# Kernel optimization log

Measured on AMD Instinct MI355X. Metric: run time of the kernel, lower is better.

The kernel has to match this reference:

```python
import jax, jax.numpy as jnp
import numpy as np

N = 100000        # num nodes
E = 3_200_000     # num edges
NFEAT, NHID, NCLASS = 256, 128, 40
BN_EPS = 1e-5


def _gcn_norm(edge_index, edge_weight, num_nodes):
    """PyG gcn_norm with self-loops (fill value 1.0): returns (src, dst, norm)."""
    loop = jnp.arange(num_nodes)
    src = jnp.concatenate([edge_index[0], loop])
    dst = jnp.concatenate([edge_index[1], loop])
    ew = jnp.concatenate([edge_weight, jnp.ones((num_nodes,), edge_weight.dtype)])
    deg = jax.ops.segment_sum(ew, dst, num_segments=num_nodes)
    dinv = jnp.where(deg > 0, jax.lax.rsqrt(jnp.maximum(deg, 1e-30)), 0.0)
    norm = dinv[src] * ew * dinv[dst]  # [E+N]
    return src, dst, norm


def _gcn_layer(h, W, b, src, dst, norm, num_nodes):
    lin = h @ W                                   # [N, out]
    msg = lin[src] * norm[:, None]                # gather + scale  [E+N, out]
    agg = jax.ops.segment_sum(msg, dst, num_segments=num_nodes)
    return agg + b


def _bn(h, gamma, beta):
    # BatchNorm1d in training mode: biased batch statistics
    m = jnp.mean(h, axis=0)
    v = jnp.mean(jnp.square(h - m), axis=0)
    return (h - m) * jax.lax.rsqrt(v + BN_EPS) * gamma + beta


def setup_inputs() -> dict:
    key = jax.random.key(0)
    ks = jax.random.split(key, 12)
    s_in = 1.0 / np.sqrt(NFEAT)
    s_h = 1.0 / np.sqrt(NHID)
    return {
        "x": jax.random.normal(ks[0], (N, NFEAT), jnp.float32),
        "edge_index": jax.random.randint(ks[1], (2, E), 0, N, dtype=jnp.int32),
        "edge_weight": jax.random.uniform(ks[2], (E,), jnp.float32),
        "W1": jax.random.normal(ks[3], (NFEAT, NHID), jnp.float32) * s_in,
        "b1": jnp.zeros((NHID,), jnp.float32),
        "g1": jnp.ones((NHID,), jnp.float32),
        "beta1": jnp.zeros((NHID,), jnp.float32),
        "W2": jax.random.normal(ks[4], (NHID, NHID), jnp.float32) * s_h,
        "b2": jnp.zeros((NHID,), jnp.float32),
        "g2": jnp.ones((NHID,), jnp.float32),
        "beta2": jnp.zeros((NHID,), jnp.float32),
        "W3": jax.random.normal(ks[5], (NHID, NHID), jnp.float32) * s_h,
        "b3": jnp.zeros((NHID,), jnp.float32),
        "g3": jnp.ones((NHID,), jnp.float32),
        "beta3": jnp.zeros((NHID,), jnp.float32),
        "linW": jax.random.normal(ks[6], (3 * NHID, NCLASS), jnp.float32) / np.sqrt(3 * NHID),
        "linb": jnp.zeros((NCLASS,), jnp.float32),
    }


def reference(x, edge_index, edge_weight,
              W1, b1, g1, beta1,
              W2, b2, g2, beta2,
              W3, b3, g3, beta3,
              linW, linb):
    src, dst, norm = _gcn_norm(edge_index, edge_weight, N)
    x1 = _bn(jax.nn.relu(_gcn_layer(x, W1, b1, src, dst, norm, N)), g1, beta1)
    x2 = _bn(jax.nn.relu(_gcn_layer(x1, W2, b2, src, dst, norm, N)), g2, beta2)
    x3 = _bn(_gcn_layer(x2, W3, b3, src, dst, norm, N), g3, beta3)  # note: no relu on x3
    embed_x = jnp.concatenate([x1, x2, x3], axis=1)  # [N, 3*NHID]
    logits = embed_x @ linW + linb                   # [N, NCLASS]
    return logits, jax.nn.softmax(logits, axis=1), embed_x
```

## Files before the change

### kernel.cpp

```cpp
#include <hip/hip_runtime.h>
#include <hip/hip_bf16.h>
#include <hip/hip_fp16.h>
#include <math.h>

#define NN 100000
#define NE 3200000
#define NF 256
#define NH 128
#define NC 40
#define BN_EPS 1e-5f

typedef __attribute__((ext_vector_type(8))) short bf16x8;
typedef __attribute__((ext_vector_type(4))) float f32x4;

__device__ __forceinline__ float2 bf2_unpack(unsigned int v) {
    return make_float2(__uint_as_float(v << 16), __uint_as_float(v & 0xffff0000u));
}
__device__ __forceinline__ unsigned int pack2bf(float lo, float hi) {
    unsigned int a = (unsigned int)__hip_bfloat16_raw(__float2bfloat16(lo)).x;
    unsigned int b = (unsigned int)__hip_bfloat16_raw(__float2bfloat16(hi)).x;
    return a | (b << 16);
}
__device__ __forceinline__ float4 affine4(float4 v, float4 sc, float4 sh) {
    v.x = fmaf(v.x, sc.x, sh.x);
    v.y = fmaf(v.y, sc.y, sh.y);
    v.z = fmaf(v.z, sc.z, sh.z);
    v.w = fmaf(v.w, sc.w, sh.w);
    return v;
}

__global__ __launch_bounds__(256) void k_init(unsigned long long* hist, float* sums) {
    int i = blockIdx.x * 256 + threadIdx.x;
    if (i < NN) hist[i] = 0ULL;
    if (i < 3 * 1024) sums[i] = 0.0f;
}

template <int K, bool BN>
__device__ __forceinline__ void gemm_body(unsigned int (*Bt)[20], const float* H, float* Hw,
                                          const float* scsh, int ldh, const float* W,
                                          __hip_bfloat16* out, int blk, int t) {
    int wid = t >> 6, l = t & 63;
    int l15 = l & 15, lhi = l >> 4;
    int rowbase = blk * 128 + wid * 32;
    int ar0 = rowbase + l15;      if (ar0 >= NN) ar0 = NN - 1;
    int ar1 = rowbase + 16 + l15; if (ar1 >= NN) ar1 = NN - 1;

    f32x4 acc[2][8];
#pragma unroll
    for (int rt = 0; rt < 2; rt++)
#pragma unroll
        for (int ct = 0; ct < 8; ct++) acc[rt][ct] = (f32x4){0.f, 0.f, 0.f, 0.f};

    for (int kb = 0; kb < K / 32; kb++) {
        __syncthreads();
        for (int i = t; i < 2048; i += 256) {
            int c = i & 127, k2l = i >> 7;
            int k = kb * 32 + 2 * k2l;
            Bt[c][k2l] = pack2bf(W[(size_t)k * NH + c], W[(size_t)(k + 1) * NH + c]);
        }
        __syncthreads();
        int kk = kb * 32 + lhi * 8;
        const float4* a0p = (const float4*)&H[(size_t)ar0 * ldh + kk];
        const float4* a1p = (const float4*)&H[(size_t)ar1 * ldh + kk];
        float4 x0 = a0p[0], x1 = a0p[1];
        float4 y0 = a1p[0], y1 = a1p[1];
        if constexpr (BN) {
            float4 sc0 = *(const float4*)&scsh[kk];
            float4 sc1 = *(const float4*)&scsh[kk + 4];
            float4 sh0 = *(const float4*)&scsh[128 + kk];
            float4 sh1 = *(const float4*)&scsh[128 + kk + 4];
            x0 = affine4(x0, sc0, sh0); x1 = affine4(x1, sc1, sh1);
            y0 = affine4(y0, sc0, sh0); y1 = affine4(y1, sc1, sh1);
            *(float4*)&Hw[(size_t)ar0 * ldh + kk] = x0;
            *(float4*)&Hw[(size_t)ar0 * ldh + kk + 4] = x1;
            *(float4*)&Hw[(size_t)ar1 * ldh + kk] = y0;
            *(float4*)&Hw[(size_t)ar1 * ldh + kk + 4] = y1;
        }
        union { unsigned int u[4]; bf16x8 v; } af0, af1;
        af0.u[0] = pack2bf(x0.x, x0.y); af0.u[1] = pack2bf(x0.z, x0.w);
        af0.u[2] = pack2bf(x1.x, x1.y); af0.u[3] = pack2bf(x1.z, x1.w);
        af1.u[0] = pack2bf(y0.x, y0.y); af1.u[1] = pack2bf(y0.z, y0.w);
        af1.u[2] = pack2bf(y1.x, y1.y); af1.u[3] = pack2bf(y1.z, y1.w);
#pragma unroll
        for (int ct = 0; ct < 8; ct++) {
            bf16x8 b = *(const bf16x8*)&Bt[ct * 16 + l15][lhi * 4];
            acc[0][ct] = __builtin_amdgcn_mfma_f32_16x16x32_bf16(af0.v, b, acc[0][ct], 0, 0, 0);
            acc[1][ct] = __builtin_amdgcn_mfma_f32_16x16x32_bf16(af1.v, b, acc[1][ct], 0, 0, 0);
        }
    }
#pragma unroll
    for (int rt = 0; rt < 2; rt++)
#pragma unroll
        for (int ct = 0; ct < 8; ct++)
#pragma unroll
            for (int reg = 0; reg < 4; reg++) {
                int row = rowbase + rt * 16 + lhi * 4 + reg;
                if (row < NN)
                    out[(size_t)row * NH + ct * 16 + l15] = __float2bfloat16(acc[rt][ct][reg]);
            }
}

__global__ __launch_bounds__(256) void k_g1edge(const float* __restrict__ x, const float* __restrict__ W1,
                                                __hip_bfloat16* __restrict__ lin,
                                                const int* __restrict__ ei, const float* __restrict__ ew,
                                                unsigned long long* __restrict__ hist,
                                                int* __restrict__ pos, int gm) {
    __shared__ unsigned int Bt[128][20];
    int t = threadIdx.x;
    int blk = (int)blockIdx.x;
    if (blk < gm) {
        gemm_body<NF, false>(Bt, x, nullptr, nullptr, NF, W1, lin, blk, t);
    } else {
        int e = (blk - gm) * 256 + t;
        if (e < NE) {
            int d = __builtin_nontemporal_load(&ei[NE + e]);
            float w = __builtin_nontemporal_load(&ew[e]);
            unsigned long long pk = (1ULL << 44) | (unsigned long long)(w * 4294967296.0f);
            unsigned long long old = atomicAdd(&hist[d], pk);
            __builtin_nontemporal_store((int)(old >> 44), &pos[e]);
        }
    }
}

__global__ __launch_bounds__(256) void k_gemm_bn(const float* H, float* Hw,
                                                 const float* __restrict__ scsh,
                                                 const float* __restrict__ W,
                                                 __hip_bfloat16* __restrict__ out) {
    __shared__ unsigned int Bt[128][20];
    gemm_body<NH, true>(Bt, H, Hw, scsh, 384, W, out, (int)blockIdx.x, (int)threadIdx.x);
}

__global__ __launch_bounds__(256) void k_dinv(const unsigned long long* __restrict__ hist,
                                              float* __restrict__ dinv) {
    int i = blockIdx.x * 256 + threadIdx.x;
    if (i < NN) {
        float ws = (float)(hist[i] & 0xFFFFFFFFFFFULL) * 2.3283064365386963e-10f;
        dinv[i] = rsqrtf(1.0f + ws);
    }
}

__global__ __launch_bounds__(1024) void k_scan(const unsigned long long* __restrict__ hist,
                                               int* __restrict__ rowptr) {
    __shared__ int wsum[16];
    __shared__ int s_carry;
    int t = threadIdx.x;
    int lane = t & 63, wid = t >> 6;
    if (t == 0) s_carry = 0;
    __syncthreads();
    for (int base = 0; base < NN; base += 4096) {
        int i0 = base + t * 4;
        int c[4];
#pragma unroll
        for (int j = 0; j < 4; j++) {
            int i = i0 + j;
            c[j] = (i < NN) ? (int)(hist[i] >> 44) : 0;
        }
        int v = c[0] + c[1] + c[2] + c[3];
        int x = v;
#pragma unroll
        for (int off = 1; off < 64; off <<= 1) {
            int y = __shfl_up(x, off);
            if (lane >= off) x += y;
        }
        if (lane == 63) wsum[wid] = x;
        __syncthreads();
        if (wid == 0 && lane < 16) {
            int s = wsum[lane];
#pragma unroll
            for (int off = 1; off < 16; off <<= 1) {
                int y = __shfl_up(s, off);
                if (lane >= off) s += y;
            }
            wsum[lane] = s;
        }
        __syncthreads();
        int woff = (wid > 0) ? wsum[wid - 1] : 0;
        int incl = x + woff;
        int carry = s_carry;
        int run = carry + incl - v;
#pragma unroll
        for (int j = 0; j < 4; j++) {
            int i = i0 + j;
            if (i < NN) rowptr[i] = run;
            run += c[j];
        }
        __syncthreads();
        if (t == 1023) s_carry = carry + incl;
        __syncthreads();
    }
    if (t == 0) rowptr[NN] = s_carry;
}

__global__ __launch_bounds__(256) void k_scatter(const int* __restrict__ ei, const float* __restrict__ ew,
                                                 const float* __restrict__ dinv,
                                                 const int* __restrict__ rowptr,
                                                 const int* __restrict__ pos,
                                                 unsigned int* __restrict__ cw) {
    int e = blockIdx.x * 256 + threadIdx.x;
    if (e >= NE) return;
    int s = __builtin_nontemporal_load(&ei[e]);
    int d = __builtin_nontemporal_load(&ei[NE + e]);
    float w = __builtin_nontemporal_load(&ew[e]);
    float nv = dinv[s] * w * dinv[d];
    unsigned int h = (unsigned int)__half_as_ushort(__float2half(nv)) & 0x7fffu;
    unsigned int packed = (unsigned int)s | (h << 17);
    int p = __builtin_nontemporal_load(&pos[e]);
    __builtin_nontemporal_store(packed, &cw[rowptr[d] + p]);
}

__global__ __launch_bounds__(256) void k_agg(const unsigned int* __restrict__ linb,
                                             const float* __restrict__ dinv,
                                             const int* __restrict__ rowptr,
                                             const unsigned int* __restrict__ cw,
                                             const float* __restrict__ bias,
                                             float* __restrict__ outp, int do_relu) {
    int t = threadIdx.x;
    int node = blockIdx.x * 4 + (t >> 6);
    if (node >= NN) return;
    int ch = t & 63;
    int c = ch << 1;
    float di = dinv[node];
    float2 sv = bf2_unpack(linb[(size_t)node * 64 + ch]);
    float a0 = fmaf(sv.x, di * di, bias[c]);
    float a1 = fmaf(sv.y, di * di, bias[c + 1]);
    int beg = rowptr[node], end = rowptr[node + 1];
    int j = beg;
    for (; j + 16 <= end; j += 16) {
        unsigned int pk[16];
#pragma unroll
        for (int q = 0; q < 16; q++) pk[q] = cw[j + q];
        unsigned int v[16];
#pragma unroll
        for (int q = 0; q < 16; q++) v[q] = linb[(size_t)(pk[q] & 0x1FFFFu) * 64 + ch];
#pragma unroll
        for (int q = 0; q < 16; q++) {
            float w = __half2float(__ushort_as_half((unsigned short)(pk[q] >> 17)));
            float2 f = bf2_unpack(v[q]);
            a0 = fmaf(f.x, w, a0);
            a1 = fmaf(f.y, w, a1);
        }
    }
    for (; j + 4 <= end; j += 4) {
        unsigned int pk[4];
#pragma unroll
        for (int q = 0; q < 4; q++) pk[q] = cw[j + q];
        unsigned int v[4];
#pragma unroll
        for (int q = 0; q < 4; q++) v[q] = linb[(size_t)(pk[q] & 0x1FFFFu) * 64 + ch];
#pragma unroll
        for (int q = 0; q < 4; q++) {
            float w = __half2float(__ushort_as_half((unsigned short)(pk[q] >> 17)));
            float2 f = bf2_unpack(v[q]);
            a0 = fmaf(f.x, w, a0);
            a1 = fmaf(f.y, w, a1);
        }
    }
    for (; j < end; j++) {
        unsigned int pk = cw[j];
        unsigned int vv = linb[(size_t)(pk & 0x1FFFFu) * 64 + ch];
        float w = __half2float(__ushort_as_half((unsigned short)(pk >> 17)));
        float2 f = bf2_unpack(vv);
        a0 = fmaf(f.x, w, a0);
        a1 = fmaf(f.y, w, a1);
    }
    if (do_relu) { a0 = fmaxf(a0, 0.f); a1 = fmaxf(a1, 0.f); }
    *(float2*)&outp[(size_t)node * 384 + c] = make_float2(a0, a1);
}

__global__ __launch_bounds__(256) void k_stats(const float* __restrict__ pre, float* __restrict__ sums) {
    int t = threadIdx.x;
    int c = t & 127, h = t >> 7;
    float s = 0.f, s2 = 0.f;
    for (int r = blockIdx.x * 2 + h; r < NN; r += gridDim.x * 2) {
        float v = pre[(size_t)r * 384 + c];
        s += v;
        s2 = fmaf(v, v, s2);
    }
    __shared__ float ls[256], ls2[256];
    ls[t] = s; ls2[t] = s2;
    __syncthreads();
    if (t < 128) {
        atomicAdd(&sums[c], ls[t] + ls[t + 128]);
        atomicAdd(&sums[NH + c], ls2[t] + ls2[t + 128]);
    }
}

__global__ void k_bnfinal(float* __restrict__ sums, const float* __restrict__ g,
                          const float* __restrict__ beta) {
    int c = threadIdx.x;
    if (c < NH) {
        float m = sums[c] * (1.0f / NN);
        float v = sums[NH + c] * (1.0f / NN) - m * m;
        float rstd = rsqrtf(v + BN_EPS);
        float sc = g[c] * rstd;
        sums[256 + c] = sc;
        sums[384 + c] = beta[c] - m * sc;
    }
}

__global__ __launch_bounds__(256) void k_final(const float* __restrict__ embed, float* embedW,
                                               const float* __restrict__ scsh3,
                                               const float* __restrict__ linW,
                                               const float* __restrict__ linb,
                                               float* __restrict__ logits, float* __restrict__ probs) {
    __shared__ unsigned int Wt[3 * 16 * 196];
    int t = threadIdx.x;
    for (int i = t; i < 3 * 16 * 192; i += 256) {
        int ct = i / (16 * 192);
        int rem = i - ct * (16 * 192);
        int c = rem / 192, k2 = rem - c * 192;
        int col = ct * 16 + c;
        float lo = (col < NC) ? linW[(size_t)(2 * k2) * NC + col] : 0.f;
        float hi = (col < NC) ? linW[(size_t)(2 * k2 + 1) * NC + col] : 0.f;
        Wt[(ct * 16 + c) * 196 + k2] = pack2bf(lo, hi);
    }
    __syncthreads();

    int wid = t >> 6, l = t & 63;
    int rowbase = blockIdx.x * 64 + wid * 16;
    int l15 = l & 15, lhi = l >> 4;

    int arow = rowbase + l15;
    if (arow > NN - 1) arow = NN - 1;
    const float4* ap = (const float4*)&embed[(size_t)arow * 384 + lhi * 8];

    f32x4 acc0 = {0.f, 0.f, 0.f, 0.f};
    f32x4 acc1 = {0.f, 0.f, 0.f, 0.f};
    f32x4 acc2 = {0.f, 0.f, 0.f, 0.f};

    for (int kb = 0; kb < 12; kb++) {
        float4 a0 = ap[kb * 8];
        float4 a1 = ap[kb * 8 + 1];
        if (kb >= 8) {
            int kk = kb * 32 + lhi * 8 - 256;
            float4 sc0 = *(const float4*)&scsh3[kk];
            float4 sc1 = *(const float4*)&scsh3[kk + 4];
            float4 sh0 = *(const float4*)&scsh3[128 + kk];
            float4 sh1 = *(const float4*)&scsh3[128 + kk + 4];
            a0 = affine4(a0, sc0, sh0);
            a1 = affine4(a1, sc1, sh1);
            *(float4*)&embedW[(size_t)arow * 384 + kb * 32 + lhi * 8] = a0;
            *(float4*)&embedW[(size_t)arow * 384 + kb * 32 + lhi * 8 + 4] = a1;
        }
        union { unsigned int u[4]; bf16x8 v; } af;
        af.u[0] = pack2bf(a0.x, a0.y);
        af.u[1] = pack2bf(a0.z, a0.w);
        af.u[2] = pack2bf(a1.x, a1.y);
        af.u[3] = pack2bf(a1.z, a1.w);
        int wbase = kb * 16 + lhi * 4;
        bf16x8 b0 = *(const bf16x8*)&Wt[(0 * 16 + l15) * 196 + wbase];
        bf16x8 b1 = *(const bf16x8*)&Wt[(1 * 16 + l15) * 196 + wbase];
        bf16x8 b2 = *(const bf16x8*)&Wt[(2 * 16 + l15) * 196 + wbase];
        acc0 = __builtin_amdgcn_mfma_f32_16x16x32_bf16(af.v, b0, acc0, 0, 0, 0);
        acc1 = __builtin_amdgcn_mfma_f32_16x16x32_bf16(af.v, b1, acc1, 0, 0, 0);
        acc2 = __builtin_amdgcn_mfma_f32_16x16x32_bf16(af.v, b2, acc2, 0, 0, 0);
    }

    int col0 = 0 * 16 + l15, col1 = 1 * 16 + l15, col2 = 2 * 16 + l15;
    float lb0 = (col0 < NC) ? linb[col0] : 0.f;
    float lb1 = (col1 < NC) ? linb[col1] : 0.f;
    float lb2 = (col2 < NC) ? linb[col2] : 0.f;

#pragma unroll
    for (int reg = 0; reg < 4; reg++) {
        int row = rowbase + lhi * 4 + reg;
        float v0 = acc0[reg] + lb0;
        float v1 = acc1[reg] + lb1;
        float v2 = acc2[reg] + lb2;
        float m = fmaxf(v0, v1);
        if (col2 < NC) m = fmaxf(m, v2);
#pragma unroll
        for (int off = 1; off < 16; off <<= 1) m = fmaxf(m, __shfl_xor(m, off));
        float e0 = __expf(v0 - m);
        float e1 = __expf(v1 - m);
        float e2 = (col2 < NC) ? __expf(v2 - m) : 0.f;
        float s = e0 + e1 + e2;
#pragma unroll
        for (int off = 1; off < 16; off <<= 1) s += __shfl_xor(s, off);
        float inv = 1.0f / s;
        if (row < NN) {
            size_t base = (size_t)row * NC;
            logits[base + col0] = v0;
            probs[base + col0] = e0 * inv;
            logits[base + col1] = v1;
            probs[base + col1] = e1 * inv;
            if (col2 < NC) {
                logits[base + col2] = v2;
                probs[base + col2] = e2 * inv;
            }
        }
    }
}

extern "C" void kernel_launch(void* const* d_in, const int* in_sizes, int n_in,
                              void* d_out, int out_size, void* d_ws, size_t ws_size,
                              hipStream_t stream) {
    const float* x    = (const float*)d_in[0];
    const int*   ei   = (const int*)d_in[1];
    const float* ew   = (const float*)d_in[2];
    const float* W1   = (const float*)d_in[3];
    const float* b1   = (const float*)d_in[4];
    const float* g1   = (const float*)d_in[5];
    const float* be1  = (const float*)d_in[6];
    const float* W2   = (const float*)d_in[7];
    const float* b2   = (const float*)d_in[8];
    const float* g2   = (const float*)d_in[9];
    const float* be2  = (const float*)d_in[10];
    const float* W3   = (const float*)d_in[11];
    const float* b3   = (const float*)d_in[12];
    const float* g3   = (const float*)d_in[13];
    const float* be3  = (const float*)d_in[14];
    const float* linW = (const float*)d_in[15];
    const float* linb = (const float*)d_in[16];

    float* out    = (float*)d_out;
    float* logits = out;
    float* probs  = out + (size_t)NN * NC;
    float* embed  = out + (size_t)2 * NN * NC;

    char* ws = (char*)d_ws;
    size_t off = 0;
    auto alloc = [&](size_t bytes) -> char* {
        char* p = ws + off;
        off = (off + bytes + 255) & ~(size_t)255;
        return p;
    };
    float*              dinv   = (float*)alloc((size_t)NN * 4);
    unsigned long long* hist   = (unsigned long long*)alloc((size_t)NN * 8);
    int*                rowptr = (int*)alloc((size_t)(NN + 1) * 4);
    unsigned int*       cw     = (unsigned int*)alloc((size_t)NE * 4);
    __hip_bfloat16*     lin    = (__hip_bfloat16*)alloc((size_t)NN * NH * 2);
    int*                pos    = (int*)alloc((size_t)NE * 4);
    float*              sums   = (float*)alloc(3 * 1024 * 4);
    (void)ws_size; (void)in_sizes; (void)n_in; (void)out_size;

    int gN = (NN + 255) / 256;
    int gE = (NE + 255) / 256;
    int gM = (NN + 127) / 128;
    int gA = (NN + 3) / 4;
    int gF = (NN + 63) / 64;

    k_init<<<gN, 256, 0, stream>>>(hist, sums);
    k_g1edge<<<gM + gE, 256, 0, stream>>>(x, W1, lin, ei, ew, hist, pos, gM);
    k_dinv<<<gN, 256, 0, stream>>>(hist, dinv);
    k_scan<<<1, 1024, 0, stream>>>(hist, rowptr);
    k_scatter<<<gE, 256, 0, stream>>>(ei, ew, dinv, rowptr, pos, cw);

    k_agg<<<gA, 256, 0, stream>>>((const unsigned int*)lin, dinv, rowptr, cw, b1, embed + 0, 1);
    k_stats<<<1024, 256, 0, stream>>>(embed + 0, sums + 0);
    k_bnfinal<<<1, 128, 0, stream>>>(sums + 0, g1, be1);
    k_gemm_bn<<<gM, 256, 0, stream>>>(embed + 0, embed + 0, sums + 256, W2, lin);
    k_agg<<<gA, 256, 0, stream>>>((const unsigned int*)lin, dinv, rowptr, cw, b2, embed + 128, 1);
    k_stats<<<1024, 256, 0, stream>>>(embed + 128, sums + 1024);
    k_bnfinal<<<1, 128, 0, stream>>>(sums + 1024, g2, be2);
    k_gemm_bn<<<gM, 256, 0, stream>>>(embed + 128, embed + 128, sums + 1024 + 256, W3, lin);
    k_agg<<<gA, 256, 0, stream>>>((const unsigned int*)lin, dinv, rowptr, cw, b3, embed + 256, 0);
    k_stats<<<1024, 256, 0, stream>>>(embed + 256, sums + 2048);
    k_bnfinal<<<1, 128, 0, stream>>>(sums + 2048, g3, be3);
    k_final<<<gF, 256, 0, stream>>>(embed, embed, sums + 2048 + 256, linW, linb, logits, probs);
}
```

Measured before the change: 989.6 us.

## Split aggregation into two channel-half passes with edge-parallel half-waves

The SpMM aggregation now runs as two launches, each covering half the 128 channels, so each pass gathers 64-byte slices of the bf16 feature rows. Within a wavefront, the two half-waves process alternating edges and combine their sums with a cross-lane shuffle. The intent is a smaller gather working set per pass, which should fit better in cache, plus more memory parallelism per node. The cost is reading the CSR edge list twice and doubling the agg launches. Separately, the dinv computation moves into the scan kernel, and the edge histogram is split out of the fused GEMM1+edge kernel so that GEMM1 runs after the scatter.

```diff
diff --git a/kernel.cpp b/kernel.cpp
--- a/kernel.cpp
+++ b/kernel.cpp
@@ -33,6 +33,93 @@
     int i = blockIdx.x * 256 + threadIdx.x;
     if (i < NN) hist[i] = 0ULL;
     if (i < 3 * 1024) sums[i] = 0.0f;
+}
+
+__global__ __launch_bounds__(256) void k_edge(const int* __restrict__ ei, const float* __restrict__ ew,
+                                              unsigned long long* __restrict__ hist,
+                                              int* __restrict__ pos) {
+    int e = blockIdx.x * 256 + threadIdx.x;
+    if (e >= NE) return;
+    int d = __builtin_nontemporal_load(&ei[NE + e]);
+    float w = __builtin_nontemporal_load(&ew[e]);
+    unsigned long long pack = (1ULL << 44) | (unsigned long long)(w * 4294967296.0f);
+    unsigned long long old = atomicAdd(&hist[d], pack);
+    __builtin_nontemporal_store((int)(old >> 44), &pos[e]);
+}
+
+__global__ __launch_bounds__(1024) void k_scan(const unsigned long long* __restrict__ hist,
+                                               int* __restrict__ rowptr,
+                                               float* __restrict__ dinv) {
+    __shared__ int wsum[16];
+    __shared__ int s_carry;
+    int t = threadIdx.x;
+    int lane = t & 63, wid = t >> 6;
+    if (t == 0) s_carry = 0;
+    __syncthreads();
+    for (int base = 0; base < NN; base += 4096) {
+        int i0 = base + t * 4;
+        int c[4];
+#pragma unroll
+        for (int j = 0; j < 4; j++) {
+            int i = i0 + j;
+            unsigned long long h = (i < NN) ? hist[i] : 0ULL;
+            c[j] = (int)(h >> 44);
+            if (i < NN) {
+                float ws = (float)(h & 0xFFFFFFFFFFFULL) * 2.3283064365386963e-10f;
+                dinv[i] = rsqrtf(1.0f + ws);
+            }
+        }
+        int v = c[0] + c[1] + c[2] + c[3];
+        int x = v;
+#pragma unroll
+        for (int off = 1; off < 64; off <<= 1) {
+            int y = __shfl_up(x, off);
+            if (lane >= off) x += y;
+        }
+        if (lane == 63) wsum[wid] = x;
+        __syncthreads();
+        if (wid == 0 && lane < 16) {
+            int s = wsum[lane];
+#pragma unroll
+            for (int off = 1; off < 16; off <<= 1) {
+                int y = __shfl_up(s, off);
+                if (lane >= off) s += y;
+            }
+            wsum[lane] = s;
+        }
+        __syncthreads();
+        int woff = (wid > 0) ? wsum[wid - 1] : 0;
+        int incl = x + woff;
+        int carry = s_carry;
+        int run = carry + incl - v;
+#pragma unroll
+        for (int j = 0; j < 4; j++) {
+            int i = i0 + j;
+            if (i < NN) rowptr[i] = run;
+            run += c[j];
+        }
+        __syncthreads();
+        if (t == 1023) s_carry = carry + incl;
+        __syncthreads();
+    }
+    if (t == 0) rowptr[NN] = s_carry;
+}
+
+__global__ __launch_bounds__(256) void k_scatter(const int* __restrict__ ei, const float* __restrict__ ew,
+                                                 const float* __restrict__ dinv,
+                                                 const int* __restrict__ rowptr,
+                                                 const int* __restrict__ pos,
+                                                 unsigned int* __restrict__ cw) {
+    int e = blockIdx.x * 256 + threadIdx.x;
+    if (e >= NE) return;
+    int s = __builtin_nontemporal_load(&ei[e]);
+    int d = __builtin_nontemporal_load(&ei[NE + e]);
+    float w = __builtin_nontemporal_load(&ew[e]);
+    float nv = dinv[s] * w * dinv[d];
+    unsigned int h = (unsigned int)__half_as_ushort(__float2half(nv)) & 0x7fffu;
+    unsigned int packed = (unsigned int)s | (h << 17);
+    int p = __builtin_nontemporal_load(&pos[e]);
+    __builtin_nontemporal_store(packed, &cw[rowptr[d] + p]);
 }
 
 template <int K, bool BN>
@@ -100,26 +187,11 @@
             }
 }
 
-__global__ __launch_bounds__(256) void k_g1edge(const float* __restrict__ x, const float* __restrict__ W1,
-                                                __hip_bfloat16* __restrict__ lin,
-                                                const int* __restrict__ ei, const float* __restrict__ ew,
-                                                unsigned long long* __restrict__ hist,
-                                                int* __restrict__ pos, int gm) {
+__global__ __launch_bounds__(256) void k_gemm1(const float* __restrict__ H,
+                                               const float* __restrict__ W,
+                                               __hip_bfloat16* __restrict__ out) {
     __shared__ unsigned int Bt[128][20];
-    int t = threadIdx.x;
-    int blk = (int)blockIdx.x;
-    if (blk < gm) {
-        gemm_body<NF, false>(Bt, x, nullptr, nullptr, NF, W1, lin, blk, t);
-    } else {
-        int e = (blk - gm) * 256 + t;
-        if (e < NE) {
-            int d = __builtin_nontemporal_load(&ei[NE + e]);
-            float w = __builtin_nontemporal_load(&ew[e]);
-            unsigned long long pk = (1ULL << 44) | (unsigned long long)(w * 4294967296.0f);
-            unsigned long long old = atomicAdd(&hist[d], pk);
-            __builtin_nontemporal_store((int)(old >> 44), &pos[e]);
-        }
-    }
+    gemm_body<NF, false>(Bt, H, nullptr, nullptr, NF, W, out, (int)blockIdx.x, (int)threadIdx.x);
 }
 
 __global__ __launch_bounds__(256) void k_gemm_bn(const float* H, float* Hw,
@@ -130,108 +202,39 @@
     gemm_body<NH, true>(Bt, H, Hw, scsh, 384, W, out, (int)blockIdx.x, (int)threadIdx.x);
 }
 
-__global__ __launch_bounds__(256) void k_dinv(const unsigned long long* __restrict__ hist,
-                                              float* __restrict__ dinv) {
-    int i = blockIdx.x * 256 + threadIdx.x;
-    if (i < NN) {
-        float ws = (float)(hist[i] & 0xFFFFFFFFFFFULL) * 2.3283064365386963e-10f;
-        dinv[i] = rsqrtf(1.0f + ws);
-    }
-}
-
-__global__ __launch_bounds__(1024) void k_scan(const unsigned long long* __restrict__ hist,
-                                               int* __restrict__ rowptr) {
-    __shared__ int wsum[16];
-    __shared__ int s_carry;
-    int t = threadIdx.x;
-    int lane = t & 63, wid = t >> 6;
-    if (t == 0) s_carry = 0;
-    __syncthreads();
-    for (int base = 0; base < NN; base += 4096) {
-        int i0 = base + t * 4;
-        int c[4];
-#pragma unroll
-        for (int j = 0; j < 4; j++) {
-            int i = i0 + j;
-            c[j] = (i < NN) ? (int)(hist[i] >> 44) : 0;
-        }
-        int v = c[0] + c[1] + c[2] + c[3];
-        int x = v;
-#pragma unroll
-        for (int off = 1; off < 64; off <<= 1) {
-            int y = __shfl_up(x, off);
-            if (lane >= off) x += y;
-        }
-        if (lane == 63) wsum[wid] = x;
-        __syncthreads();
-        if (wid == 0 && lane < 16) {
-            int s = wsum[lane];
-#pragma unroll
-            for (int off = 1; off < 16; off <<= 1) {
-                int y = __shfl_up(s, off);
-                if (lane >= off) s += y;
-            }
-            wsum[lane] = s;
-        }
-        __syncthreads();
-        int woff = (wid > 0) ? wsum[wid - 1] : 0;
-        int incl = x + woff;
-        int carry = s_carry;
-        int run = carry + incl - v;
-#pragma unroll
-        for (int j = 0; j < 4; j++) {
-            int i = i0 + j;
-            if (i < NN) rowptr[i] = run;
-            run += c[j];
-        }
-        __syncthreads();
-        if (t == 1023) s_carry = carry + incl;
-        __syncthreads();
-    }
-    if (t == 0) rowptr[NN] = s_carry;
-}
-
-__global__ __launch_bounds__(256) void k_scatter(const int* __restrict__ ei, const float* __restrict__ ew,
-                                                 const float* __restrict__ dinv,
-                                                 const int* __restrict__ rowptr,
-                                                 const int* __restrict__ pos,
-                                                 unsigned int* __restrict__ cw) {
-    int e = blockIdx.x * 256 + threadIdx.x;
-    if (e >= NE) return;
-    int s = __builtin_nontemporal_load(&ei[e]);
-    int d = __builtin_nontemporal_load(&ei[NE + e]);
-    float w = __builtin_nontemporal_load(&ew[e]);
-    float nv = dinv[s] * w * dinv[d];
-    unsigned int h = (unsigned int)__half_as_ushort(__float2half(nv)) & 0x7fffu;
-    unsigned int packed = (unsigned int)s | (h << 17);
-    int p = __builtin_nontemporal_load(&pos[e]);
-    __builtin_nontemporal_store(packed, &cw[rowptr[d] + p]);
-}
-
-__global__ __launch_bounds__(256) void k_agg(const unsigned int* __restrict__ linb,
-                                             const float* __restrict__ dinv,
-                                             const int* __restrict__ rowptr,
-                                             const unsigned int* __restrict__ cw,
-                                             const float* __restrict__ bias,
-                                             float* __restrict__ outp, int do_relu) {
+template <int PASS>
+__global__ __launch_bounds__(256) void k_agg_h(const unsigned int* __restrict__ linb,
+                                               const float* __restrict__ dinv,
+                                               const int* __restrict__ rowptr,
+                                               const unsigned int* __restrict__ cw,
+                                               const float* __restrict__ bias,
+                                               float* __restrict__ outp, int do_relu) {
     int t = threadIdx.x;
     int node = blockIdx.x * 4 + (t >> 6);
     if (node >= NN) return;
-    int ch = t & 63;
-    int c = ch << 1;
-    float di = dinv[node];
-    float2 sv = bf2_unpack(linb[(size_t)node * 64 + ch]);
-    float a0 = fmaf(sv.x, di * di, bias[c]);
-    float a1 = fmaf(sv.y, di * di, bias[c + 1]);
+    int lane = t & 63;
+    int epar = lane >> 5;
+    int ch32 = lane & 31;
+    int c = PASS * 64 + (ch32 << 1);
+    float a0, a1;
+    if (epar == 0) {
+        float di = dinv[node];
+        float2 sv = bf2_unpack(linb[(size_t)node * 64 + PASS * 32 + ch32]);
+        a0 = fmaf(sv.x, di * di, bias[c]);
+        a1 = fmaf(sv.y, di * di, bias[c + 1]);
+    } else {
+        a0 = 0.f; a1 = 0.f;
+    }
     int beg = rowptr[node], end = rowptr[node + 1];
     int j = beg;
-    for (; j + 16 <= end; j += 16) {
+    for (; j + 32 <= end; j += 32) {
         unsigned int pk[16];
 #pragma unroll
-        for (int q = 0; q < 16; q++) pk[q] = cw[j + q];
+        for (int q = 0; q < 16; q++) pk[q] = cw[j + 2 * q + epar];
         unsigned int v[16];
 #pragma unroll
-        for (int q = 0; q < 16; q++) v[q] = linb[(size_t)(pk[q] & 0x1FFFFu) * 64 + ch];
+        for (int q = 0; q < 16; q++)
+            v[q] = linb[(size_t)(pk[q] & 0x1FFFFu) * 64 + PASS * 32 + ch32];
 #pragma unroll
         for (int q = 0; q < 16; q++) {
             float w = __half2float(__ushort_as_half((unsigned short)(pk[q] >> 17)));
@@ -240,31 +243,28 @@
             a1 = fmaf(f.y, w, a1);
         }
     }
-    for (; j + 4 <= end; j += 4) {
-        unsigned int pk[4];
-#pragma unroll
-        for (int q = 0; q < 4; q++) pk[q] = cw[j + q];
-        unsigned int v[4];
-#pragma unroll
-        for (int q = 0; q < 4; q++) v[q] = linb[(size_t)(pk[q] & 0x1FFFFu) * 64 + ch];
-#pragma unroll
-        for (int q = 0; q < 4; q++) {
-            float w = __half2float(__ushort_as_half((unsigned short)(pk[q] >> 17)));
-            float2 f = bf2_unpack(v[q]);
-            a0 = fmaf(f.x, w, a0);
-            a1 = fmaf(f.y, w, a1);
-        }
-    }
-    for (; j < end; j++) {
-        unsigned int pk = cw[j];
-        unsigned int vv = linb[(size_t)(pk & 0x1FFFFu) * 64 + ch];
+    for (; j + 2 <= end; j += 2) {
+        unsigned int pk = cw[j + epar];
+        unsigned int vv = linb[(size_t)(pk & 0x1FFFFu) * 64 + PASS * 32 + ch32];
         float w = __half2float(__ushort_as_half((unsigned short)(pk >> 17)));
         float2 f = bf2_unpack(vv);
         a0 = fmaf(f.x, w, a0);
         a1 = fmaf(f.y, w, a1);
     }
-    if (do_relu) { a0 = fmaxf(a0, 0.f); a1 = fmaxf(a1, 0.f); }
-    *(float2*)&outp[(size_t)node * 384 + c] = make_float2(a0, a1);
+    if (j < end && epar == 0) {
+        unsigned int pk = cw[j];
+        unsigned int vv = linb[(size_t)(pk & 0x1FFFFu) * 64 + PASS * 32 + ch32];
+        float w = __half2float(__ushort_as_half((unsigned short)(pk >> 17)));
+        float2 f = bf2_unpack(vv);
+        a0 = fmaf(f.x, w, a0);
+        a1 = fmaf(f.y, w, a1);
+    }
+    a0 += __shfl_xor(a0, 32);
+    a1 += __shfl_xor(a1, 32);
+    if (epar == 0) {
+        if (do_relu) { a0 = fmaxf(a0, 0.f); a1 = fmaxf(a1, 0.f); }
+        *(float2*)&outp[(size_t)node * 384 + c] = make_float2(a0, a1);
+    }
 }
 
 __global__ __launch_bounds__(256) void k_stats(const float* __restrict__ pre, float* __restrict__ sums) {
@@ -441,20 +441,23 @@
     int gF = (NN + 63) / 64;
 
     k_init<<<gN, 256, 0, stream>>>(hist, sums);
-    k_g1edge<<<gM + gE, 256, 0, stream>>>(x, W1, lin, ei, ew, hist, pos, gM);
-    k_dinv<<<gN, 256, 0, stream>>>(hist, dinv);
-    k_scan<<<1, 1024, 0, stream>>>(hist, rowptr);
+    k_edge<<<gE, 256, 0, stream>>>(ei, ew, hist, pos);
+    k_scan<<<1, 1024, 0, stream>>>(hist, rowptr, dinv);
     k_scatter<<<gE, 256, 0, stream>>>(ei, ew, dinv, rowptr, pos, cw);
 
-    k_agg<<<gA, 256, 0, stream>>>((const unsigned int*)lin, dinv, rowptr, cw, b1, embed + 0, 1);
+    k_gemm1<<<gM, 256, 0, stream>>>(x, W1, lin);
+    k_agg_h<0><<<gA, 256, 0, stream>>>((const unsigned int*)lin, dinv, rowptr, cw, b1, embed + 0, 1);
+    k_agg_h<1><<<gA, 256, 0, stream>>>((const unsigned int*)lin, dinv, rowptr, cw, b1, embed + 0, 1);
     k_stats<<<1024, 256, 0, stream>>>(embed + 0, sums + 0);
     k_bnfinal<<<1, 128, 0, stream>>>(sums + 0, g1, be1);
     k_gemm_bn<<<gM, 256, 0, stream>>>(embed + 0, embed + 0, sums + 256, W2, lin);
-    k_agg<<<gA, 256, 0, stream>>>((const unsigned int*)lin, dinv, rowptr, cw, b2, embed + 128, 1);
+    k_agg_h<0><<<gA, 256, 0, stream>>>((const unsigned int*)lin, dinv, rowptr, cw, b2, embed + 128, 1);
+    k_agg_h<1><<<gA, 256, 0, stream>>>((const unsigned int*)lin, dinv, rowptr, cw, b2, embed + 128, 1);
     k_stats<<<1024, 256, 0, stream>>>(embed + 128, sums + 1024);
     k_bnfinal<<<1, 128, 0, stream>>>(sums + 1024, g2, be2);
     k_gemm_bn<<<gM, 256, 0, stream>>>(embed + 128, embed + 128, sums + 1024 + 256, W3, lin);
-    k_agg<<<gA, 256, 0, stream>>>((const unsigned int*)lin, dinv, rowptr, cw, b3, embed + 256, 0);
+    k_agg_h<0><<<gA, 256, 0, stream>>>((const unsigned int*)lin, dinv, rowptr, cw, b3, embed + 256, 0);
+    k_agg_h<1><<<gA, 256, 0, stream>>>((const unsigned int*)lin, dinv, rowptr, cw, b3, embed + 256, 0);
     k_stats<<<1024, 256, 0, stream>>>(embed + 256, sums + 2048);
     k_bnfinal<<<1, 128, 0, stream>>>(sums + 2048, g3, be3);
     k_final<<<gF, 256, 0, stream>>>(embed, embed, sums + 2048 + 256, linW, linb, logits, probs);
```

Result: slower. 1.342 ms (+35.7%).

## Split fused GEMM1/edge-histogram kernel and fold dinv into single-block scan

Applied to the files above, without the earlier changes.

Undoes the fusion of the first GEMM with the edge histogram pass. The histogram now runs as its own kernel and the GEMM1 launch moves to after the scatter. The dinv computation is merged into the single-block scan kernel, which removes one launch. The costs are losing the overlap of the GEMM with the atomic-bound edge pass, and running the rsqrt work on a single block in the serial scan.

```diff
diff --git a/kernel.cpp b/kernel.cpp
--- a/kernel.cpp
+++ b/kernel.cpp
@@ -33,6 +33,93 @@
     int i = blockIdx.x * 256 + threadIdx.x;
     if (i < NN) hist[i] = 0ULL;
     if (i < 3 * 1024) sums[i] = 0.0f;
+}
+
+__global__ __launch_bounds__(256) void k_edge(const int* __restrict__ ei, const float* __restrict__ ew,
+                                              unsigned long long* __restrict__ hist,
+                                              int* __restrict__ pos) {
+    int e = blockIdx.x * 256 + threadIdx.x;
+    if (e >= NE) return;
+    int d = __builtin_nontemporal_load(&ei[NE + e]);
+    float w = __builtin_nontemporal_load(&ew[e]);
+    unsigned long long pack = (1ULL << 44) | (unsigned long long)(w * 4294967296.0f);
+    unsigned long long old = atomicAdd(&hist[d], pack);
+    __builtin_nontemporal_store((int)(old >> 44), &pos[e]);
+}
+
+__global__ __launch_bounds__(1024) void k_scan(const unsigned long long* __restrict__ hist,
+                                               int* __restrict__ rowptr,
+                                               float* __restrict__ dinv) {
+    __shared__ int wsum[16];
+    __shared__ int s_carry;
+    int t = threadIdx.x;
+    int lane = t & 63, wid = t >> 6;
+    if (t == 0) s_carry = 0;
+    __syncthreads();
+    for (int base = 0; base < NN; base += 4096) {
+        int i0 = base + t * 4;
+        int c[4];
+#pragma unroll
+        for (int j = 0; j < 4; j++) {
+            int i = i0 + j;
+            unsigned long long h = (i < NN) ? hist[i] : 0ULL;
+            c[j] = (int)(h >> 44);
+            if (i < NN) {
+                float ws = (float)(h & 0xFFFFFFFFFFFULL) * 2.3283064365386963e-10f;
+                dinv[i] = rsqrtf(1.0f + ws);
+            }
+        }
+        int v = c[0] + c[1] + c[2] + c[3];
+        int x = v;
+#pragma unroll
+        for (int off = 1; off < 64; off <<= 1) {
+            int y = __shfl_up(x, off);
+            if (lane >= off) x += y;
+        }
+        if (lane == 63) wsum[wid] = x;
+        __syncthreads();
+        if (wid == 0 && lane < 16) {
+            int s = wsum[lane];
+#pragma unroll
+            for (int off = 1; off < 16; off <<= 1) {
+                int y = __shfl_up(s, off);
+                if (lane >= off) s += y;
+            }
+            wsum[lane] = s;
+        }
+        __syncthreads();
+        int woff = (wid > 0) ? wsum[wid - 1] : 0;
+        int incl = x + woff;
+        int carry = s_carry;
+        int run = carry + incl - v;
+#pragma unroll
+        for (int j = 0; j < 4; j++) {
+            int i = i0 + j;
+            if (i < NN) rowptr[i] = run;
+            run += c[j];
+        }
+        __syncthreads();
+        if (t == 1023) s_carry = carry + incl;
+        __syncthreads();
+    }
+    if (t == 0) rowptr[NN] = s_carry;
+}
+
+__global__ __launch_bounds__(256) void k_scatter(const int* __restrict__ ei, const float* __restrict__ ew,
+                                                 const float* __restrict__ dinv,
+                                                 const int* __restrict__ rowptr,
+                                                 const int* __restrict__ pos,
+                                                 unsigned int* __restrict__ cw) {
+    int e = blockIdx.x * 256 + threadIdx.x;
+    if (e >= NE) return;
+    int s = __builtin_nontemporal_load(&ei[e]);
+    int d = __builtin_nontemporal_load(&ei[NE + e]);
+    float w = __builtin_nontemporal_load(&ew[e]);
+    float nv = dinv[s] * w * dinv[d];
+    unsigned int h = (unsigned int)__half_as_ushort(__float2half(nv)) & 0x7fffu;
+    unsigned int packed = (unsigned int)s | (h << 17);
+    int p = __builtin_nontemporal_load(&pos[e]);
+    __builtin_nontemporal_store(packed, &cw[rowptr[d] + p]);
 }
 
 template <int K, bool BN>
@@ -100,26 +187,11 @@
             }
 }
 
-__global__ __launch_bounds__(256) void k_g1edge(const float* __restrict__ x, const float* __restrict__ W1,
-                                                __hip_bfloat16* __restrict__ lin,
-                                                const int* __restrict__ ei, const float* __restrict__ ew,
-                                                unsigned long long* __restrict__ hist,
-                                                int* __restrict__ pos, int gm) {
+__global__ __launch_bounds__(256) void k_gemm1(const float* __restrict__ H,
+                                               const float* __restrict__ W,
+                                               __hip_bfloat16* __restrict__ out) {
     __shared__ unsigned int Bt[128][20];
-    int t = threadIdx.x;
-    int blk = (int)blockIdx.x;
-    if (blk < gm) {
-        gemm_body<NF, false>(Bt, x, nullptr, nullptr, NF, W1, lin, blk, t);
-    } else {
-        int e = (blk - gm) * 256 + t;
-        if (e < NE) {
-            int d = __builtin_nontemporal_load(&ei[NE + e]);
-            float w = __builtin_nontemporal_load(&ew[e]);
-            unsigned long long pk = (1ULL << 44) | (unsigned long long)(w * 4294967296.0f);
-            unsigned long long old = atomicAdd(&hist[d], pk);
-            __builtin_nontemporal_store((int)(old >> 44), &pos[e]);
-        }
-    }
+    gemm_body<NF, false>(Bt, H, nullptr, nullptr, NF, W, out, (int)blockIdx.x, (int)threadIdx.x);
 }
 
 __global__ __launch_bounds__(256) void k_gemm_bn(const float* H, float* Hw,
@@ -128,84 +200,6 @@
                                                  __hip_bfloat16* __restrict__ out) {
     __shared__ unsigned int Bt[128][20];
     gemm_body<NH, true>(Bt, H, Hw, scsh, 384, W, out, (int)blockIdx.x, (int)threadIdx.x);
-}
-
-__global__ __launch_bounds__(256) void k_dinv(const unsigned long long* __restrict__ hist,
-                                              float* __restrict__ dinv) {
-    int i = blockIdx.x * 256 + threadIdx.x;
-    if (i < NN) {
-        float ws = (float)(hist[i] & 0xFFFFFFFFFFFULL) * 2.3283064365386963e-10f;
-        dinv[i] = rsqrtf(1.0f + ws);
-    }
-}
-
-__global__ __launch_bounds__(1024) void k_scan(const unsigned long long* __restrict__ hist,
-                                               int* __restrict__ rowptr) {
-    __shared__ int wsum[16];
-    __shared__ int s_carry;
-    int t = threadIdx.x;
-    int lane = t & 63, wid = t >> 6;
-    if (t == 0) s_carry = 0;
-    __syncthreads();
-    for (int base = 0; base < NN; base += 4096) {
-        int i0 = base + t * 4;
-        int c[4];
-#pragma unroll
-        for (int j = 0; j < 4; j++) {
-            int i = i0 + j;
-            c[j] = (i < NN) ? (int)(hist[i] >> 44) : 0;
-        }
-        int v = c[0] + c[1] + c[2] + c[3];
-        int x = v;
-#pragma unroll
-        for (int off = 1; off < 64; off <<= 1) {
-            int y = __shfl_up(x, off);
-            if (lane >= off) x += y;
-        }
-        if (lane == 63) wsum[wid] = x;
-        __syncthreads();
-        if (wid == 0 && lane < 16) {
-            int s = wsum[lane];
-#pragma unroll
-            for (int off = 1; off < 16; off <<= 1) {
-                int y = __shfl_up(s, off);
-                if (lane >= off) s += y;
-            }
-            wsum[lane] = s;
-        }
-        __syncthreads();
-        int woff = (wid > 0) ? wsum[wid - 1] : 0;
-        int incl = x + woff;
-        int carry = s_carry;
-        int run = carry + incl - v;
-#pragma unroll
-        for (int j = 0; j < 4; j++) {
-            int i = i0 + j;
-            if (i < NN) rowptr[i] = run;
-            run += c[j];
-        }
-        __syncthreads();
-        if (t == 1023) s_carry = carry + incl;
-        __syncthreads();
-    }
-    if (t == 0) rowptr[NN] = s_carry;
-}
-
-__global__ __launch_bounds__(256) void k_scatter(const int* __restrict__ ei, const float* __restrict__ ew,
-                                                 const float* __restrict__ dinv,
-                                                 const int* __restrict__ rowptr,
-                                                 const int* __restrict__ pos,
-                                                 unsigned int* __restrict__ cw) {
-    int e = blockIdx.x * 256 + threadIdx.x;
-    if (e >= NE) return;
-    int s = __builtin_nontemporal_load(&ei[e]);
-    int d = __builtin_nontemporal_load(&ei[NE + e]);
-    float w = __builtin_nontemporal_load(&ew[e]);
-    float nv = dinv[s] * w * dinv[d];
-    unsigned int h = (unsigned int)__half_as_ushort(__float2half(nv)) & 0x7fffu;
-    unsigned int packed = (unsigned int)s | (h << 17);
-    int p = __builtin_nontemporal_load(&pos[e]);
-    __builtin_nontemporal_store(packed, &cw[rowptr[d] + p]);
 }
 
 __global__ __launch_bounds__(256) void k_agg(const unsigned int* __restrict__ linb,
@@ -441,11 +435,11 @@
     int gF = (NN + 63) / 64;
 
     k_init<<<gN, 256, 0, stream>>>(hist, sums);
-    k_g1edge<<<gM + gE, 256, 0, stream>>>(x, W1, lin, ei, ew, hist, pos, gM);
-    k_dinv<<<gN, 256, 0, stream>>>(hist, dinv);
-    k_scan<<<1, 1024, 0, stream>>>(hist, rowptr);
+    k_edge<<<gE, 256, 0, stream>>>(ei, ew, hist, pos);
+    k_scan<<<1, 1024, 0, stream>>>(hist, rowptr, dinv);
     k_scatter<<<gE, 256, 0, stream>>>(ei, ew, dinv, rowptr, pos, cw);
 
+    k_gemm1<<<gM, 256, 0, stream>>>(x, W1, lin);
     k_agg<<<gA, 256, 0, stream>>>((const unsigned int*)lin, dinv, rowptr, cw, b1, embed + 0, 1);
     k_stats<<<1024, 256, 0, stream>>>(embed + 0, sums + 0);
     k_bnfinal<<<1, 128, 0, stream>>>(sums + 0, g1, be1);
```

New measurement: 1.028 ms. 3.9% more time.
